# Kernel tuning notes

Measured on AMD Instinct MI355X. Metric: run time of the kernel, lower is better.

The kernel has to match this reference:

```python
import jax, jax.numpy as jnp
import numpy as np
from jax.scipy.linalg import solve_triangular

OMEGA = 1.5  # params_fix['omega']
BS, N, MAXITER = 512, 256, 200
RTOL = 1e-6


def setup_inputs() -> dict:
    key = jax.random.key(0)
    k1, k2, k3 = jax.random.split(key, 3)
    # diagonally dominant A so SOR converges
    A = jax.random.normal(k1, (BS, N, N), jnp.float32) + N * jnp.eye(N, dtype=jnp.float32)
    b = jax.random.normal(k2, (BS, N), jnp.float32)
    x_sol = jnp.linalg.solve(A, b[..., None])[..., 0]
    theta = jax.random.normal(k3, (BS, N), jnp.float32)  # initial iterate x0
    rtol = jnp.full((BS,), RTOL, jnp.float32)
    return {"A": A, "b": b, "x_sol": x_sol, "theta": theta, "rtol": rtol, "maxiter": MAXITER}


def reference(A, b, x_sol, theta, rtol, maxiter):
    bs, n, _ = A.shape
    b = b.reshape(bs, n, 1)
    x0 = theta.reshape(bs, n, 1)
    xs = x_sol.reshape(bs, n, 1)

    diag = jnp.diagonal(A, axis1=1, axis2=2)          # [bs, n]
    D = jnp.eye(n, dtype=A.dtype) * diag[:, :, None]  # diag_embed
    L = jnp.tril(A, -1)
    U = jnp.triu(A, 1)

    omega = jnp.asarray(OMEGA, A.dtype)
    G1 = D + omega * L                      # lower triangular, [bs, n, n]
    G2 = omega * U + (omega - 1.0) * D
    G = solve_triangular(G1, -G2, lower=True)        # iteration matrix
    f = solve_triangular(G1, omega * b, lower=True)  # affine term

    err0 = jnp.linalg.norm(xs - x0, axis=(1, 2))     # [bs]
    xtol = jnp.linalg.norm(xs, axis=(1, 2)) * rtol   # [bs]

    def step(carry, _):
        x, err, done = carry
        # global stopping criterion: while any(err > xtol)
        done = jnp.logical_or(done, jnp.logical_not(jnp.any(err > xtol)))
        x_new = jnp.where(done, x, G @ x + f)
        err_new = jnp.where(done, err, jnp.linalg.norm(xs - x_new, axis=(1, 2)))
        hist = jnp.where(done, jnp.zeros_like(err), err_new)  # unwritten slots stay 0
        return (x_new, err_new, done), hist

    init = (x0, err0, jnp.asarray(False))
    _, hist = jax.lax.scan(step, init, None, length=maxiter)  # hist: [maxiter, bs]
    return jnp.concatenate([err0[:, None], hist.T], axis=1)   # [bs, maxiter+1]
```

## Files before the change

kernel.cpp:

```cpp
#include <hip/hip_runtime.h>
#include <math.h>

#define BS 512
#define NN 256
#define RB 16
#define OMEGA_F 1.5f

__global__ __launch_bounds__(512, 1) void sor_fused(
    const float* __restrict__ A,
    const float* __restrict__ xs,
    const float* __restrict__ x0,
    const float* __restrict__ rtol,
    const int* __restrict__ maxiter_p,
    float* __restrict__ out)
{
    const int b   = blockIdx.x;
    const int tid = threadIdx.x;
    const int t   = tid & 255;
    const int q   = tid >> 8;
    const int qU  = __builtin_amdgcn_readfirstlane(q);
    const int w   = __builtin_amdgcn_readfirstlane(tid >> 6);
    const int u   = tid & 63;
    const float* __restrict__ Ab = A + (size_t)b * NN * NN;

    __shared__ __align__(16) char smem[65536];
    float (*ldsA)[NN]    = (float (*)[NN])(smem);
    float (*acc2)[NN]    = (float (*)[NN])(smem + 16384);
    float (*xbuf)[NN]    = (float (*)[NN])(smem + 32768);
    float (*ldsX)[NN]    = (float (*)[NN])(smem);
    float* rs            = (float*)(smem + 16384);
    float* e             = (float*)(smem);
    float (*pbuf)[4][64] = (float (*)[4][64])(smem + 1024);
    float* nrm           = (float*)(smem + 1024 + 8192);

    const int mi = *maxiter_p;
    float* __restrict__ outb = out + (size_t)b * (mi + 1);

    float ev = 0.f;
    if (q == 0) {
        const float xsv = xs[b * NN + t];
        ev = xsv - x0[b * NN + t];
        float s1 = ev * ev, s2 = xsv * xsv;
        #pragma unroll
        for (int off = 32; off > 0; off >>= 1) {
            s1 += __shfl_down(s1, off);
            s2 += __shfl_down(s2, off);
        }
        if ((t & 63) == 0) { rs[t >> 6] = s1; rs[4 + (t >> 6)] = s2; }
    }
    __syncthreads();
    const float err0 = sqrtf(rs[0] + rs[1] + rs[2] + rs[3]);
    const float xtol = sqrtf(rs[4] + rs[5] + rs[6] + rs[7]) * rtol[b];
    if (tid == 0) outb[0] = err0;

    float g[8][RB];
    for (int KB = 0; KB < NN / RB; ++KB) {
        const int r0 = KB * RB;
        __syncthreads();
        #pragma unroll
        for (int i = 0; i < 2; ++i) {
            const int lin = tid + 512 * i;
            const int rr = lin >> 6, c4 = (lin & 63) << 2;
            *(float4*)&ldsA[rr][c4] = *(const float4*)&Ab[(size_t)(r0 + rr) * NN + c4];
        }
        __syncthreads();

        float acc[RB];
        #pragma unroll
        for (int rr = 0; rr < RB; ++rr) acc[rr] = 0.f;
        #pragma unroll
        for (int m = 0; m < 8; ++m) {
            const int kb = 2 * m + qU;
            if (kb < KB) {
                const int j0 = kb * RB;
                #pragma unroll
                for (int jw = 0; jw < 4; ++jw) {
                    const float g0 = g[m][4 * jw + 0];
                    const float g1 = g[m][4 * jw + 1];
                    const float g2 = g[m][4 * jw + 2];
                    const float g3 = g[m][4 * jw + 3];
                    #pragma unroll
                    for (int hc = 0; hc < 4; ++hc) {
                        float4 a_[4];
                        #pragma unroll
                        for (int h = 0; h < 4; ++h)
                            a_[h] = *(const float4*)&Ab[(size_t)(r0 + 4 * hc + h) * NN + j0 + 4 * jw];
                        #pragma unroll
                        for (int h = 0; h < 4; ++h)
                            acc[4 * hc + h] += a_[h].x * g0 + a_[h].y * g1
                                             + a_[h].z * g2 + a_[h].w * g3;
                    }
                }
            }
        }
        if (q == 1) {
            #pragma unroll
            for (int rr = 0; rr < RB; ++rr) acc2[rr][t] = acc[rr];
        }
        __syncthreads();
        if (q == 0) {
            float s_[RB];
            #pragma unroll
            for (int rr = 0; rr < RB; ++rr) s_[rr] = acc[rr] + acc2[rr][t];
            #pragma unroll
            for (int rr = 0; rr < RB; ++rr) {
                const int r = r0 + rr;
                const float a_rt = ldsA[rr][t];
                const float brt  = (t > r) ? (-OMEGA_F) * a_rt
                                 : ((t == r) ? (1.0f - OMEGA_F) * a_rt : 0.0f);
                const float diag = ldsA[rr][r];
                const float val  = (brt - OMEGA_F * s_[rr]) / diag;
                xbuf[rr][t] = val;
                #pragma unroll
                for (int rr2 = rr + 1; rr2 < RB; ++rr2)
                    s_[rr2] += ldsA[rr2][r] * val;
            }
        }
        __syncthreads();
        if ((KB & 1) == q) {
            const int m = KB >> 1;
            #pragma unroll
            for (int rr = 0; rr < RB; ++rr) g[m][rr] = xbuf[rr][t];
        }
    }

    float4 gi[4][8];
    #pragma unroll
    for (int R = 0; R < 4; ++R) {
        __syncthreads();
        #pragma unroll
        for (int i = 0; i < 2; ++i) {
            #pragma unroll
            for (int rr = 0; rr < RB; ++rr) {
                const int lr = (2 * i + q) * RB + rr;
                ldsX[lr][(t + 4 * lr) & 255] = g[2 * R + i][rr];
            }
        }
        __syncthreads();
        #pragma unroll
        for (int jj4 = 0; jj4 < 8; ++jj4) {
            const int c = 32 * w + 4 * jj4;
            gi[R][jj4] = *(const float4*)&ldsX[u][(c + 4 * u) & 255];
        }
    }
    __syncthreads();

    if (tid < NN) e[tid] = ev;
    __syncthreads();

    const float4* __restrict__ e4 = (const float4*)e;
    float err = err0;
    int s = 1;
    for (; s <= mi; ++s) {
        if (!(err > xtol)) break;
        float a0 = 0.f, a1 = 0.f, a2 = 0.f, a3 = 0.f;
        #pragma unroll
        for (int jj4 = 0; jj4 < 8; ++jj4) {
            const float4 ev4 = e4[8 * w + jj4];
            a0 += gi[0][jj4].x*ev4.x + gi[0][jj4].y*ev4.y + gi[0][jj4].z*ev4.z + gi[0][jj4].w*ev4.w;
            a1 += gi[1][jj4].x*ev4.x + gi[1][jj4].y*ev4.y + gi[1][jj4].z*ev4.z + gi[1][jj4].w*ev4.w;
            a2 += gi[2][jj4].x*ev4.x + gi[2][jj4].y*ev4.y + gi[2][jj4].z*ev4.z + gi[2][jj4].w*ev4.w;
            a3 += gi[3][jj4].x*ev4.x + gi[3][jj4].y*ev4.y + gi[3][jj4].z*ev4.z + gi[3][jj4].w*ev4.w;
        }
        pbuf[w][0][u] = a0;
        pbuf[w][1][u] = a1;
        pbuf[w][2][u] = a2;
        pbuf[w][3][u] = a3;
        __syncthreads();
        if (tid < NN) {
            const int kk = tid >> 6, uu = tid & 63;
            float sum = 0.f;
            #pragma unroll
            for (int w2 = 0; w2 < 8; ++w2) sum += pbuf[w2][kk][uu];
            e[tid] = sum;
            float loc = sum * sum;
            #pragma unroll
            for (int off = 32; off > 0; off >>= 1) loc += __shfl_down(loc, off);
            if (uu == 0) nrm[kk] = loc;
        }
        __syncthreads();
        err = sqrtf(nrm[0] + nrm[1] + nrm[2] + nrm[3]);
        if (tid == 0) outb[s] = err;
    }
    for (int idx = s + tid; idx <= mi; idx += 512) outb[idx] = 0.f;
}

extern "C" void kernel_launch(void* const* d_in, const int* in_sizes, int n_in,
                              void* d_out, int out_size, void* d_ws, size_t ws_size,
                              hipStream_t stream) {
    const float* A     = (const float*)d_in[0];
    const float* xs    = (const float*)d_in[2];
    const float* theta = (const float*)d_in[3];
    const float* rtol  = (const float*)d_in[4];
    const int*   mi    = (const int*)d_in[5];
    float* out = (float*)d_out;

    sor_fused<<<dim3(BS), dim3(512), 0, stream>>>(
        A, xs, theta, rtol, mi, out);
}
```

Baseline: 609.9 us.

## Split fused SOR kernel into triangular-solve and iteration kernels via workspace

```diff
diff --git a/kernel.cpp b/kernel.cpp
--- a/kernel.cpp
+++ b/kernel.cpp
@@ -6,8 +6,111 @@
 #define RB 16
 #define OMEGA_F 1.5f
 
-__global__ __launch_bounds__(512, 1) void sor_fused(
+
+__global__ __launch_bounds__(512) void sor_solve(
     const float* __restrict__ A,
+    float4* __restrict__ arr)
+{
+    const int b   = blockIdx.x;
+    const int tid = threadIdx.x;
+    const int t2  = tid & 127;
+    const int q   = tid >> 7;
+    const int qU  = __builtin_amdgcn_readfirstlane(q);
+    const float* __restrict__ Ab   = A + (size_t)b * NN * NN;
+    float4* __restrict__       arrB = arr + (size_t)b * (NN / 4) * NN;
+
+    __shared__ __align__(16) char smem[57344];
+    float (*ldsA)[NN]      = (float (*)[NN])(smem);
+    float (*bufs)[RB][128] = (float (*)[RB][128])(smem + 16384);
+    float (*xbuf)[128]     = (float (*)[128])(smem + 40960);
+
+    for (int p = 0; p < 2; ++p) {
+        const int c = p * 128 + t2;
+        float g[4][RB];
+
+        for (int KB = 0; KB < NN / RB; ++KB) {
+            const int r0 = KB * RB;
+            __syncthreads();
+            #pragma unroll
+            for (int i = 0; i < 2; ++i) {
+                const int lin = tid + 512 * i;
+                const int rr = lin >> 6, c4 = (lin & 63) << 2;
+                *(float4*)&ldsA[rr][c4] = *(const float4*)&Ab[(size_t)(r0 + rr) * NN + c4];
+            }
+            __syncthreads();
+
+            float acc[RB];
+            #pragma unroll
+            for (int rr = 0; rr < RB; ++rr) acc[rr] = 0.f;
+            #pragma unroll
+            for (int m = 0; m < 4; ++m) {
+                const int kb = 4 * m + qU;
+                if (kb < KB) {
+                    const int j0 = kb * RB;
+                    #pragma unroll
+                    for (int jw = 0; jw < 4; ++jw) {
+                        const float g0 = g[m][4 * jw + 0];
+                        const float g1 = g[m][4 * jw + 1];
+                        const float g2 = g[m][4 * jw + 2];
+                        const float g3 = g[m][4 * jw + 3];
+                        #pragma unroll
+                        for (int hc = 0; hc < 4; ++hc) {
+                            float4 a_[4];
+                            #pragma unroll
+                            for (int h = 0; h < 4; ++h)
+                                a_[h] = *(const float4*)&Ab[(size_t)(r0 + 4 * hc + h) * NN + j0 + 4 * jw];
+                            #pragma unroll
+                            for (int h = 0; h < 4; ++h)
+                                acc[4 * hc + h] += a_[h].x * g0 + a_[h].y * g1
+                                                 + a_[h].z * g2 + a_[h].w * g3;
+                        }
+                    }
+                }
+            }
+            if (q >= 1) {
+                #pragma unroll
+                for (int rr = 0; rr < RB; ++rr) bufs[q - 1][rr][t2] = acc[rr];
+            }
+            __syncthreads();
+            if (q == 0) {
+                float s_[RB];
+                #pragma unroll
+                for (int rr = 0; rr < RB; ++rr)
+                    s_[rr] = acc[rr] + bufs[0][rr][t2] + bufs[1][rr][t2] + bufs[2][rr][t2];
+                #pragma unroll
+                for (int rr = 0; rr < RB; ++rr) {
+                    const int r = r0 + rr;
+                    const float a_rc = ldsA[rr][c];
+                    const float brc  = (c > r) ? (-OMEGA_F) * a_rc
+                                     : ((c == r) ? (1.0f - OMEGA_F) * a_rc : 0.0f);
+                    const float diag = ldsA[rr][r];
+                    const float val  = (brc - OMEGA_F * s_[rr]) / diag;
+                    xbuf[rr][t2] = val;
+                    #pragma unroll
+                    for (int rr2 = rr + 1; rr2 < RB; ++rr2)
+                        s_[rr2] += ldsA[rr2][r] * val;
+                }
+            }
+            __syncthreads();
+            #pragma unroll
+            for (int m = 0; m < 4; ++m) {
+                if (KB == 4 * m + q) {
+                    #pragma unroll
+                    for (int rr = 0; rr < RB; ++rr) g[m][rr] = xbuf[rr][t2];
+                }
+            }
+            {
+                const int rr  = tid & 15;
+                const int j4l = tid >> 4;
+                const float4 v = *(const float4*)&xbuf[rr][4 * j4l];
+                arrB[(size_t)(p * 32 + j4l) * NN + r0 + rr] = v;
+            }
+        }
+    }
+}
+
+__global__ __launch_bounds__(1024) void sor_iterate(
+    const float4* __restrict__ arr,
     const float* __restrict__ xs,
     const float* __restrict__ x0,
     const float* __restrict__ rtol,
@@ -16,173 +119,66 @@
 {
     const int b   = blockIdx.x;
     const int tid = threadIdx.x;
-    const int t   = tid & 255;
-    const int q   = tid >> 8;
-    const int qU  = __builtin_amdgcn_readfirstlane(q);
-    const int w   = __builtin_amdgcn_readfirstlane(tid >> 6);
-    const int u   = tid & 63;
-    const float* __restrict__ Ab = A + (size_t)b * NN * NN;
+    const int r   = tid & 255;
+    const int qq  = tid >> 8;
+    const int qqU = __builtin_amdgcn_readfirstlane(qq);
+    const float4* __restrict__ arrB = arr + (size_t)b * (NN / 4) * NN;
 
-    __shared__ __align__(16) char smem[65536];
-    float (*ldsA)[NN]    = (float (*)[NN])(smem);
-    float (*acc2)[NN]    = (float (*)[NN])(smem + 16384);
-    float (*xbuf)[NN]    = (float (*)[NN])(smem + 32768);
-    float (*ldsX)[NN]    = (float (*)[NN])(smem);
-    float* rs            = (float*)(smem + 16384);
-    float* e             = (float*)(smem);
-    float (*pbuf)[4][64] = (float (*)[4][64])(smem + 1024);
-    float* nrm           = (float*)(smem + 1024 + 8192);
+    __shared__ __align__(16) char smem[86016];
+    float* e           = (float*)smem;
+    float (*pbuf)[NN]  = (float (*)[NN])(smem + 1024);
+    float* nrm         = (float*)(smem + 1024 + 4096);
+
+    float4 gq[16];
+    #pragma unroll
+    for (int k = 0; k < 16; ++k)
+        gq[k] = arrB[(size_t)(qqU * 16 + k) * NN + r];
 
     const int mi = *maxiter_p;
     float* __restrict__ outb = out + (size_t)b * (mi + 1);
 
-    float ev = 0.f;
-    if (q == 0) {
-        const float xsv = xs[b * NN + t];
-        ev = xsv - x0[b * NN + t];
+    if (tid < NN) {
+        const float xsv = xs[b * NN + tid];
+        const float ev  = xsv - x0[b * NN + tid];
+        e[tid] = ev;
         float s1 = ev * ev, s2 = xsv * xsv;
         #pragma unroll
         for (int off = 32; off > 0; off >>= 1) {
             s1 += __shfl_down(s1, off);
             s2 += __shfl_down(s2, off);
         }
-        if ((t & 63) == 0) { rs[t >> 6] = s1; rs[4 + (t >> 6)] = s2; }
+        if ((tid & 63) == 0) { nrm[tid >> 6] = s1; nrm[4 + (tid >> 6)] = s2; }
     }
     __syncthreads();
-    const float err0 = sqrtf(rs[0] + rs[1] + rs[2] + rs[3]);
-    const float xtol = sqrtf(rs[4] + rs[5] + rs[6] + rs[7]) * rtol[b];
+    const float err0 = sqrtf(nrm[0] + nrm[1] + nrm[2] + nrm[3]);
+    const float xtol = sqrtf(nrm[4] + nrm[5] + nrm[6] + nrm[7]) * rtol[b];
     if (tid == 0) outb[0] = err0;
 
-    float g[8][RB];
-    for (int KB = 0; KB < NN / RB; ++KB) {
-        const int r0 = KB * RB;
-        __syncthreads();
-        #pragma unroll
-        for (int i = 0; i < 2; ++i) {
-            const int lin = tid + 512 * i;
-            const int rr = lin >> 6, c4 = (lin & 63) << 2;
-            *(float4*)&ldsA[rr][c4] = *(const float4*)&Ab[(size_t)(r0 + rr) * NN + c4];
-        }
-        __syncthreads();
-
-        float acc[RB];
-        #pragma unroll
-        for (int rr = 0; rr < RB; ++rr) acc[rr] = 0.f;
-        #pragma unroll
-        for (int m = 0; m < 8; ++m) {
-            const int kb = 2 * m + qU;
-            if (kb < KB) {
-                const int j0 = kb * RB;
-                #pragma unroll
-                for (int jw = 0; jw < 4; ++jw) {
-                    const float g0 = g[m][4 * jw + 0];
-                    const float g1 = g[m][4 * jw + 1];
-                    const float g2 = g[m][4 * jw + 2];
-                    const float g3 = g[m][4 * jw + 3];
-                    #pragma unroll
-                    for (int hc = 0; hc < 4; ++hc) {
-                        float4 a_[4];
-                        #pragma unroll
-                        for (int h = 0; h < 4; ++h)
-                            a_[h] = *(const float4*)&Ab[(size_t)(r0 + 4 * hc + h) * NN + j0 + 4 * jw];
-                        #pragma unroll
-                        for (int h = 0; h < 4; ++h)
-                            acc[4 * hc + h] += a_[h].x * g0 + a_[h].y * g1
-                                             + a_[h].z * g2 + a_[h].w * g3;
-                    }
-                }
-            }
-        }
-        if (q == 1) {
-            #pragma unroll
-            for (int rr = 0; rr < RB; ++rr) acc2[rr][t] = acc[rr];
-        }
-        __syncthreads();
-        if (q == 0) {
-            float s_[RB];
-            #pragma unroll
-            for (int rr = 0; rr < RB; ++rr) s_[rr] = acc[rr] + acc2[rr][t];
-            #pragma unroll
-            for (int rr = 0; rr < RB; ++rr) {
-                const int r = r0 + rr;
-                const float a_rt = ldsA[rr][t];
-                const float brt  = (t > r) ? (-OMEGA_F) * a_rt
-                                 : ((t == r) ? (1.0f - OMEGA_F) * a_rt : 0.0f);
-                const float diag = ldsA[rr][r];
-                const float val  = (brt - OMEGA_F * s_[rr]) / diag;
-                xbuf[rr][t] = val;
-                #pragma unroll
-                for (int rr2 = rr + 1; rr2 < RB; ++rr2)
-                    s_[rr2] += ldsA[rr2][r] * val;
-            }
-        }
-        __syncthreads();
-        if ((KB & 1) == q) {
-            const int m = KB >> 1;
-            #pragma unroll
-            for (int rr = 0; rr < RB; ++rr) g[m][rr] = xbuf[rr][t];
-        }
-    }
-
-    float4 gi[4][8];
-    #pragma unroll
-    for (int R = 0; R < 4; ++R) {
-        __syncthreads();
-        #pragma unroll
-        for (int i = 0; i < 2; ++i) {
-            #pragma unroll
-            for (int rr = 0; rr < RB; ++rr) {
-                const int lr = (2 * i + q) * RB + rr;
-                ldsX[lr][(t + 4 * lr) & 255] = g[2 * R + i][rr];
-            }
-        }
-        __syncthreads();
-        #pragma unroll
-        for (int jj4 = 0; jj4 < 8; ++jj4) {
-            const int c = 32 * w + 4 * jj4;
-            gi[R][jj4] = *(const float4*)&ldsX[u][(c + 4 * u) & 255];
-        }
-    }
-    __syncthreads();
-
-    if (tid < NN) e[tid] = ev;
-    __syncthreads();
-
-    const float4* __restrict__ e4 = (const float4*)e;
     float err = err0;
     int s = 1;
     for (; s <= mi; ++s) {
         if (!(err > xtol)) break;
-        float a0 = 0.f, a1 = 0.f, a2 = 0.f, a3 = 0.f;
+        float a = 0.f;
         #pragma unroll
-        for (int jj4 = 0; jj4 < 8; ++jj4) {
-            const float4 ev4 = e4[8 * w + jj4];
-            a0 += gi[0][jj4].x*ev4.x + gi[0][jj4].y*ev4.y + gi[0][jj4].z*ev4.z + gi[0][jj4].w*ev4.w;
-            a1 += gi[1][jj4].x*ev4.x + gi[1][jj4].y*ev4.y + gi[1][jj4].z*ev4.z + gi[1][jj4].w*ev4.w;
-            a2 += gi[2][jj4].x*ev4.x + gi[2][jj4].y*ev4.y + gi[2][jj4].z*ev4.z + gi[2][jj4].w*ev4.w;
-            a3 += gi[3][jj4].x*ev4.x + gi[3][jj4].y*ev4.y + gi[3][jj4].z*ev4.z + gi[3][jj4].w*ev4.w;
+        for (int k = 0; k < 16; ++k) {
+            const float4 e4 = *(const float4*)&e[qqU * 64 + 4 * k];
+            a += gq[k].x * e4.x + gq[k].y * e4.y + gq[k].z * e4.z + gq[k].w * e4.w;
         }
-        pbuf[w][0][u] = a0;
-        pbuf[w][1][u] = a1;
-        pbuf[w][2][u] = a2;
-        pbuf[w][3][u] = a3;
+        pbuf[qq][r] = a;
         __syncthreads();
         if (tid < NN) {
-            const int kk = tid >> 6, uu = tid & 63;
-            float sum = 0.f;
-            #pragma unroll
-            for (int w2 = 0; w2 < 8; ++w2) sum += pbuf[w2][kk][uu];
+            const float sum = pbuf[0][tid] + pbuf[1][tid] + pbuf[2][tid] + pbuf[3][tid];
             e[tid] = sum;
             float loc = sum * sum;
             #pragma unroll
             for (int off = 32; off > 0; off >>= 1) loc += __shfl_down(loc, off);
-            if (uu == 0) nrm[kk] = loc;
+            if ((tid & 63) == 0) nrm[tid >> 6] = loc;
         }
         __syncthreads();
         err = sqrtf(nrm[0] + nrm[1] + nrm[2] + nrm[3]);
         if (tid == 0) outb[s] = err;
     }
-    for (int idx = s + tid; idx <= mi; idx += 512) outb[idx] = 0.f;
+    for (int idx = s + tid; idx <= mi; idx += 1024) outb[idx] = 0.f;
 }
 
 extern "C" void kernel_launch(void* const* d_in, const int* in_sizes, int n_in,
@@ -195,6 +191,9 @@
     const int*   mi    = (const int*)d_in[5];
     float* out = (float*)d_out;
 
-    sor_fused<<<dim3(BS), dim3(512), 0, stream>>>(
-        A, xs, theta, rtol, mi, out);
+    float4* arr = (float4*)d_ws;
+
+    sor_solve<<<dim3(BS), dim3(512), 0, stream>>>(A, arr);
+    sor_iterate<<<dim3(BS), dim3(1024), 0, stream>>>(
+        arr, xs, theta, rtol, mi, out);
 }
```

Result: slower. 659.6 us (+8.2%).
